# Optimization experiments

Measured on AMD Instinct MI355X. Metric: run time of the kernel, lower is better.

## Reference

```python
import jax, jax.numpy as jnp
import numpy as np

N, DIN = 8192, 768
DH1, DO1 = 64, 64
DH2, DO2 = 32, 64


def setup_inputs() -> dict:
    key = jax.random.key(0)
    ks = jax.random.split(key, 12)
    s = lambda *sh: 0.02
    inp = {
        "X": jax.random.normal(ks[0], (N, DIN), jnp.float32),
        "A": jax.random.randint(ks[1], (N, N), 0, 2, jnp.int32),
        # GAT layer 1: W (din->dh), a (2dh), W2 (dh->dout) + bias
        "W1": jax.random.normal(ks[2], (DIN, DH1), jnp.float32) * 0.02,
        "a1": jax.random.normal(ks[3], (2 * DH1,), jnp.float32) * 0.02,
        "W21": jax.random.normal(ks[4], (DH1, DO1), jnp.float32) * 0.02,
        "b21": jnp.zeros((DO1,), jnp.float32),
        # GAT layer 2
        "Wg2": jax.random.normal(ks[5], (DO1, DH2), jnp.float32) * 0.02,
        "a2": jax.random.normal(ks[6], (2 * DH2,), jnp.float32) * 0.02,
        "W22": jax.random.normal(ks[7], (DH2, DO2), jnp.float32) * 0.02,
        "b22": jnp.zeros((DO2,), jnp.float32),
        # MLP head: 64 -> 64 -> 2
        "M1": jax.random.normal(ks[8], (DO2, 64), jnp.float32) * 0.02,
        "bm1": jnp.zeros((64,), jnp.float32),
        "M2": jax.random.normal(ks[9], (64, 2), jnp.float32) * 0.02,
        "bm2": jnp.zeros((2,), jnp.float32),
    }
    return inp


def _tiny_gat(X, A, W, a, W2, b2):
    # H = X @ W; e_ij = a . [H_i, H_j] = H_i@a_src + H_j@a_dst (same math,
    # no N x N x 2dh intermediate)
    H = X @ W                      # [N, dh]
    dh = W.shape[1]
    e = (H @ a[:dh])[:, None] + (H @ a[dh:])[None, :]   # [N, N]
    e = jnp.where(A == 0, jnp.float32(-1e9), e)
    alpha = jax.nn.softmax(e, axis=1)                   # softmax over neighbors j
    Z = alpha @ H                                       # [N, dh]
    return jax.nn.elu(Z @ W2 + b2)


def reference(X, A, W1, a1, W21, b21, Wg2, a2, W22, b22, M1, bm1, M2, bm2):
    Z = _tiny_gat(X, A, W1, a1, W21, b21)    # [N, 64]
    Z = _tiny_gat(Z, A, Wg2, a2, W22, b22)   # [N, 64]
    g = Z.mean(axis=0)                       # [64]
    h = jax.nn.relu(g @ M1 + bm1)
    return h @ M2 + bm2                      # [2]
```

## Files before the change

### kernel.cpp

```cpp
#include <hip/hip_runtime.h>


#define NN 8192

typedef __attribute__((ext_vector_type(8))) short s16x8;
typedef __attribute__((ext_vector_type(4))) float f32x4;
union V16 { uint4 u; s16x8 s; };

static constexpr size_t OFF_WBITS = 0;
static constexpr size_t OFF_GT1H  = (size_t)8 << 20;
static constexpr size_t OFF_GT1L  = (size_t)9 << 20;
static constexpr size_t OFF_U1    = (size_t)10 << 20;
static constexpr size_t OFF_DEN1  = ((size_t)10 << 20) + 32 * 1024;
static constexpr size_t OFF_GT2H  = ((size_t)10 << 20) + 128 * 1024;
static constexpr size_t OFF_GT2L  = ((size_t)10 << 20) + 896 * 1024;
static constexpr size_t OFF_GPART = ((size_t)11 << 20) + 768 * 1024;
static constexpr size_t OFF_NUMP  = (size_t)12 << 20;
static constexpr size_t OFF_WTAH  = (size_t)44 << 20;
static constexpr size_t OFF_WTAL  = ((size_t)44 << 20) + 128 * 1024;
static constexpr size_t OFF_DP    = (size_t)45 << 20;

__device__ __forceinline__ float elu_f(float x) {
    return x > 0.f ? x : expm1f(x);
}
__device__ __forceinline__ unsigned int bf16_rne(float x) {
    unsigned int u = __float_as_uint(x);
    return (u + 0x7FFFu + ((u >> 16) & 1u)) >> 16;
}
__device__ __forceinline__ unsigned int split_pack(float g) {
    unsigned int hi = bf16_rne(g);
    float fhi = __uint_as_float(hi << 16);
    unsigned int lo = bf16_rne(g - fhi);
    return (hi << 16) | lo;
}
__device__ __forceinline__ void split3(float f, unsigned int& h, unsigned int& m,
                                       unsigned int& l) {
    h = bf16_rne(f);
    float fh = __uint_as_float(h << 16);
    float r1 = f - fh;
    m = bf16_rne(r1);
    float fm = __uint_as_float(m << 16);
    l = bf16_rne(r1 - fm);
}
__device__ __forceinline__ unsigned int bits2bf(unsigned int b2) {
    return (b2 & 1u) * 0x3F80u + (b2 & 2u) * 0x1FC00000u;
}

__global__ __launch_bounds__(256) void k_wsetup(const float* __restrict__ W1,
                                                unsigned int* __restrict__ WtAh,
                                                unsigned int* __restrict__ WtAl) {
    const int t = blockIdx.x * 256 + threadIdx.x;
    const int tile = t >> 6, lane = t & 63;
    const int mt = tile / 24, kt = tile % 24;
    const int feat = mt * 16 + (lane & 15), quad = lane >> 4;
    uint4 hv, lv;
    unsigned int h0, l0, h1, l1;
#define WQ(Q, F)                                                        \
    {                                                                   \
        int k0 = kt * 32 + quad * 8 + 2 * Q;                            \
        float w0 = W1[(size_t)k0 * 64 + feat];                          \
        float w1 = W1[(size_t)(k0 + 1) * 64 + feat];                    \
        h0 = bf16_rne(w0); l0 = bf16_rne(w0 - __uint_as_float(h0 << 16));\
        h1 = bf16_rne(w1); l1 = bf16_rne(w1 - __uint_as_float(h1 << 16));\
        hv.F = h0 | (h1 << 16);                                         \
        lv.F = l0 | (l1 << 16);                                         \
    }
    WQ(0, x) WQ(1, y) WQ(2, z) WQ(3, w)
#undef WQ
    size_t base = (size_t)((mt * 24 + kt) * 64 + lane) * 4;
    *(uint4*)(WtAh + base) = hv;
    *(uint4*)(WtAl + base) = lv;
}

__global__ __launch_bounds__(256) void k_xw1m(const float* __restrict__ X,
                                              const unsigned int* __restrict__ WtAh,
                                              const unsigned int* __restrict__ WtAl,
                                              float* __restrict__ Dp) {
    const int tid = threadIdx.x, wv = tid >> 6, lane = tid & 63;
    const int n = lane & 15, quad = lane >> 4;
    const int node = blockIdx.x * 64 + wv * 16 + n;
    const int ntg = blockIdx.x * 4 + wv;
    const int ks = blockIdx.y;
    f32x4 acc[4];
#pragma unroll
    for (int mt = 0; mt < 4; ++mt) acc[mt] = (f32x4){0.f, 0.f, 0.f, 0.f};
    const float4* X4 = (const float4*)X;
    for (int kk = 0; kk < 6; ++kk) {
        const int kt = ks * 6 + kk;
        float4 x01 = X4[(size_t)node * 192 + kt * 8 + quad * 2];
        float4 x23 = X4[(size_t)node * 192 + kt * 8 + quad * 2 + 1];
        float xf[8] = {x01.x, x01.y, x01.z, x01.w, x23.x, x23.y, x23.z, x23.w};
        V16 bh, bm, bl;
        unsigned int* bhp = (unsigned int*)&bh.u;
        unsigned int* bmp = (unsigned int*)&bm.u;
        unsigned int* blp = (unsigned int*)&bl.u;
#pragma unroll
        for (int q = 0; q < 4; ++q) {
            unsigned int h0, m0, l0, h1, m1, l1;
            split3(xf[2 * q], h0, m0, l0);
            split3(xf[2 * q + 1], h1, m1, l1);
            bhp[q] = h0 | (h1 << 16);
            bmp[q] = m0 | (m1 << 16);
            blp[q] = l0 | (l1 << 16);
        }
#pragma unroll
        for (int mt = 0; mt < 4; ++mt) {
            size_t base = (size_t)((mt * 24 + kt) * 64 + lane) * 4;
            V16 awh, awl;
            awh.u = *(const uint4*)(WtAh + base);
            awl.u = *(const uint4*)(WtAl + base);
            acc[mt] = __builtin_amdgcn_mfma_f32_16x16x32_bf16(awh.s, bh.s, acc[mt], 0, 0, 0);
            acc[mt] = __builtin_amdgcn_mfma_f32_16x16x32_bf16(awh.s, bm.s, acc[mt], 0, 0, 0);
            acc[mt] = __builtin_amdgcn_mfma_f32_16x16x32_bf16(awh.s, bl.s, acc[mt], 0, 0, 0);
            acc[mt] = __builtin_amdgcn_mfma_f32_16x16x32_bf16(awl.s, bh.s, acc[mt], 0, 0, 0);
            acc[mt] = __builtin_amdgcn_mfma_f32_16x16x32_bf16(awl.s, bm.s, acc[mt], 0, 0, 0);
        }
    }
#pragma unroll
    for (int mt = 0; mt < 4; ++mt)
        *(f32x4*)&Dp[(size_t)(((ks * 4 + mt) * 512 + ntg) * 64 + lane) * 4] = acc[mt];
}

__global__ __launch_bounds__(256) void k_xcomb(const float* __restrict__ Dp,
                                               const float* __restrict__ a1,
                                               unsigned int* __restrict__ Gt1h,
                                               unsigned int* __restrict__ Gt1l,
                                               float* __restrict__ u1) {
    __shared__ float Hsh[64][33];
    __shared__ float us[32];
    const int tid = threadIdx.x;
    if (tid < 128) {
        const int ntl = tid >> 6, lane = tid & 63;
        const int n = lane & 15, quad = lane >> 4;
        const int ntg = blockIdx.x * 2 + ntl;
        float dpart = 0.f;
#pragma unroll
        for (int mt = 0; mt < 4; ++mt) {
            float v[4] = {0.f, 0.f, 0.f, 0.f};
#pragma unroll
            for (int ksp = 0; ksp < 4; ++ksp) {
                const float* p = &Dp[(size_t)(((ksp * 4 + mt) * 512 + ntg) * 64 + lane) * 4];
                v[0] += p[0]; v[1] += p[1]; v[2] += p[2]; v[3] += p[3];
            }
#pragma unroll
            for (int r = 0; r < 4; ++r) {
                int feat = mt * 16 + quad * 4 + r;
                Hsh[feat][ntl * 16 + n] = v[r];
                dpart += v[r] * a1[64 + feat];
            }
        }
        dpart += __shfl_xor(dpart, 16);
        dpart += __shfl_xor(dpart, 32);
        float uu = expf(dpart);
        if (lane < 16) {
            us[ntl * 16 + lane] = uu;
            u1[blockIdx.x * 32 + ntl * 16 + lane] = uu;
        }
    }
    __syncthreads();
    {
        const int mt = tid >> 6, lane = tid & 63;
        const int feat = mt * 16 + (lane & 15), quad = lane >> 4;
        uint4 hv, lv;
        unsigned int g0, g1;
#define PACK_Q(Q, FX)                                                   \
        {                                                               \
            int j0 = quad * 8 + 2 * Q;                                  \
            g0 = split_pack(us[j0] * Hsh[feat][j0]);                    \
            g1 = split_pack(us[j0 + 1] * Hsh[feat][j0 + 1]);            \
            hv.FX = (g0 >> 16) | (g1 & 0xFFFF0000u);                    \
            lv.FX = (g0 & 0xFFFFu) | (g1 << 16);                        \
        }
        PACK_Q(0, x) PACK_Q(1, y) PACK_Q(2, z) PACK_Q(3, w)
#undef PACK_Q
        size_t base = ((size_t)(mt * 256 + blockIdx.x) * 64 + lane) * 4;
        *(uint4*)(Gt1h + base) = hv;
        *(uint4*)(Gt1l + base) = lv;
    }
}

__global__ __launch_bounds__(256) void k_pack(const int* __restrict__ A,
                                              const float* __restrict__ u1,
                                              unsigned int* __restrict__ Wb32,
                                              float* __restrict__ den1) {
    __shared__ unsigned short msh[8][512];
    const int tid = threadIdx.x, wv = tid >> 6, lane = tid & 63;
    const int row0 = blockIdx.x * 8;
    float dsum0 = 0.f, dsum1 = 0.f;
    const int r0 = row0 + wv * 2, r1 = r0 + 1;
    for (int c = 0; c < 8; ++c) {
        const int j = c * 1024 + lane * 16;
        const int4* A0 = (const int4*)(A + (size_t)r0 * NN + j);
        const int4* A1 = (const int4*)(A + (size_t)r1 * NN + j);
        const float4* U4 = (const float4*)(u1 + j);
        int4 a0 = A0[0], a1 = A0[1], a2 = A0[2], a3 = A0[3];
        int4 b0 = A1[0], b1 = A1[1], b2 = A1[2], b3 = A1[3];
        float4 u0 = U4[0], u4 = U4[1], u8 = U4[2], uc = U4[3];
        unsigned int m0 = 0, m1 = 0;
#define DO4(AV, BV, UV, SH)                                            \
        m0 |= ((AV.x != 0) << (SH)) | ((AV.y != 0) << (SH + 1)) |      \
              ((AV.z != 0) << (SH + 2)) | ((AV.w != 0) << (SH + 3));   \
        m1 |= ((BV.x != 0) << (SH)) | ((BV.y != 0) << (SH + 1)) |      \
              ((BV.z != 0) << (SH + 2)) | ((BV.w != 0) << (SH + 3));   \
        dsum0 += (AV.x != 0 ? UV.x : 0.f) + (AV.y != 0 ? UV.y : 0.f) + \
                 (AV.z != 0 ? UV.z : 0.f) + (AV.w != 0 ? UV.w : 0.f);  \
        dsum1 += (BV.x != 0 ? UV.x : 0.f) + (BV.y != 0 ? UV.y : 0.f) + \
                 (BV.z != 0 ? UV.z : 0.f) + (BV.w != 0 ? UV.w : 0.f);
        DO4(a0, b0, u0, 0) DO4(a1, b1, u4, 4) DO4(a2, b2, u8, 8) DO4(a3, b3, uc, 12)
#undef DO4
        msh[wv * 2 + 0][c * 64 + lane] = (unsigned short)m0;
        msh[wv * 2 + 1][c * 64 + lane] = (unsigned short)m1;
    }
#pragma unroll
    for (int off = 32; off; off >>= 1) {
        dsum0 += __shfl_down(dsum0, off);
        dsum1 += __shfl_down(dsum1, off);
    }
    if (lane == 0) { den1[r0] = dsum0; den1[r1] = dsum1; }
    __syncthreads();
    {
        const int r = tid >> 5, i = tid & 31;
        const uint4* src = (const uint4*)&msh[r][0];
        uint4* dst = (uint4*)(Wb32 + (size_t)(row0 + r) * 256);
        dst[i] = src[i];
        dst[i + 32] = src[i + 32];
    }
}

__global__ __launch_bounds__(256) void k_attn1(const unsigned int* __restrict__ Wb32,
                                               const unsigned int* __restrict__ Gt1h,
                                               const unsigned int* __restrict__ Gt1l,
                                               float* __restrict__ num1p) {
    __shared__ unsigned int bw[64 * 20];
    const int tid = threadIdx.x, wv = tid >> 6, lane = tid & 63;
    const int node0 = blockIdx.x * 64;
    const int kt0 = blockIdx.y * 16;
    {
        const int r = tid >> 2, part = tid & 3;
        const uint4* src = (const uint4*)(Wb32 + (size_t)(node0 + r) * 256 + kt0 + part * 4);
        *(uint4*)&bw[r * 20 + part * 4] = src[0];
    }
    __syncthreads();
    const int n = lane & 15, quad = lane >> 4;
    const int mt = wv;
    f32x4 acc[4];
#pragma unroll
    for (int nt = 0; nt < 4; ++nt) acc[nt] = (f32x4){0.f, 0.f, 0.f, 0.f};
#pragma unroll 4
    for (int ks = 0; ks < 16; ++ks) {
        size_t base = ((size_t)(mt * 256 + kt0 + ks) * 64 + lane) * 4;
        V16 ah, al;
        ah.u = *(const uint4*)(Gt1h + base);
        al.u = *(const uint4*)(Gt1l + base);
#pragma unroll
        for (int nt = 0; nt < 4; ++nt) {
            unsigned int by8 = (bw[(nt * 16 + n) * 20 + ks] >> (quad * 8)) & 0xFFu;
            V16 bf;
            bf.u = make_uint4(bits2bf(by8), bits2bf(by8 >> 2),
                              bits2bf(by8 >> 4), bits2bf(by8 >> 6));
            acc[nt] = __builtin_amdgcn_mfma_f32_16x16x32_bf16(ah.s, bf.s, acc[nt], 0, 0, 0);
            acc[nt] = __builtin_amdgcn_mfma_f32_16x16x32_bf16(al.s, bf.s, acc[nt], 0, 0, 0);
        }
    }
    const int s = blockIdx.y;
#pragma unroll
    for (int nt = 0; nt < 4; ++nt) {
        const int node = node0 + nt * 16 + n;
        *(f32x4*)&num1p[((size_t)s * NN + node) * 64 + mt * 16 + quad * 4] = acc[nt];
    }
}

__global__ __launch_bounds__(512) void k_ep1(const float* __restrict__ num1p,
                                             const float* __restrict__ den1,
                                             const float* __restrict__ W21,
                                             const float* __restrict__ b21,
                                             const float* __restrict__ Wg2,
                                             const float* __restrict__ a2,
                                             unsigned int* __restrict__ Gt2h,
                                             unsigned int* __restrict__ Gt2l) {
    __shared__ float w21sh[64 * 64];
    __shared__ float wg2sh[64 * 32];
    __shared__ float zsh[8][64];
    __shared__ float osh[8][64];
    __shared__ unsigned int g2sh[32][33];
    __shared__ unsigned int u2sh[32];
    const int tid = threadIdx.x, wv = tid >> 6, lane = tid & 63;
    const int node0 = blockIdx.x * 32;
    {
        const float4* s4 = (const float4*)W21;
        float4* d4 = (float4*)w21sh;
        d4[tid] = s4[tid];
        d4[tid + 512] = s4[tid + 512];
        ((float4*)wg2sh)[tid] = ((const float4*)Wg2)[tid];
    }
    const float bb = b21[lane];
    const int l32 = lane & 31;
    const float a2v = (lane < 32) ? a2[32 + l32] : 0.f;
    __syncthreads();
    for (int it = 0; it < 4; ++it) {
        const int node = node0 + wv * 4 + it;
        float sacc = 0.f;
#pragma unroll
        for (int sp = 0; sp < 16; ++sp)
            sacc += num1p[((size_t)sp * NN + node) * 64 + lane];
        zsh[wv][lane] = sacc / den1[node];
        __builtin_amdgcn_wave_barrier();
        float o0 = 0.f, o1 = 0.f, o2 = 0.f, o3 = 0.f;
        for (int c = 0; c < 64; c += 4) {
            o0 += zsh[wv][c + 0] * w21sh[(c + 0) * 64 + lane];
            o1 += zsh[wv][c + 1] * w21sh[(c + 1) * 64 + lane];
            o2 += zsh[wv][c + 2] * w21sh[(c + 2) * 64 + lane];
            o3 += zsh[wv][c + 3] * w21sh[(c + 3) * 64 + lane];
        }
        float o = elu_f(bb + ((o0 + o1) + (o2 + o3)));
        osh[wv][lane] = o;
        __builtin_amdgcn_wave_barrier();
        float h0 = 0.f, h1 = 0.f;
        for (int c = 0; c < 64; c += 2) {
            h0 += osh[wv][c + 0] * wg2sh[(c + 0) * 32 + l32];
            h1 += osh[wv][c + 1] * wg2sh[(c + 1) * 32 + l32];
        }
        float hval = h0 + h1;
        float pp = hval * a2v;
#pragma unroll
        for (int off = 32; off; off >>= 1) pp += __shfl_down(pp, off);
        float d2 = __shfl(pp, 0);
        float uu = expf(d2);
        const int nodeloc = wv * 4 + it;
        if (lane == 0) u2sh[nodeloc] = split_pack(uu);
        if (lane < 32) g2sh[l32][nodeloc] = split_pack(uu * hval);
    }
    __syncthreads();
    if (tid < 192) {
        const int mt = tid >> 6, lane2 = tid & 63;
        const int ml = lane2 & 15, quad = lane2 >> 4;
        uint4 hv, lv;
        unsigned int g0, g1;
#define PACK_Q(Q, F)                                                   \
        {                                                              \
            int j0 = quad * 8 + 2 * Q;                                 \
            if (mt < 2) { g0 = g2sh[mt * 16 + ml][j0];                 \
                          g1 = g2sh[mt * 16 + ml][j0 + 1]; }           \
            else if (ml == 0) { g0 = u2sh[j0]; g1 = u2sh[j0 + 1]; }    \
            else { g0 = 0; g1 = 0; }                                   \
            hv.F = (g0 >> 16) | (g1 & 0xFFFF0000u);                    \
            lv.F = (g0 & 0xFFFFu) | (g1 << 16);                        \
        }
        PACK_Q(0, x) PACK_Q(1, y) PACK_Q(2, z) PACK_Q(3, w)
#undef PACK_Q
        size_t base = ((size_t)(mt * 256 + blockIdx.x) * 64 + lane2) * 4;
        *(uint4*)(Gt2h + base) = hv;
        *(uint4*)(Gt2l + base) = lv;
    }
}

__global__ __launch_bounds__(256) void k_attn2(const unsigned int* __restrict__ Wb32,
                                               const unsigned int* __restrict__ Gt2h,
                                               const unsigned int* __restrict__ Gt2l,
                                               float* __restrict__ num2p) {
    __shared__ unsigned int bw[64 * 20];
    const int tid = threadIdx.x, wv = tid >> 6, lane = tid & 63;
    const int node0 = blockIdx.x * 64;
    const int kt0 = blockIdx.y * 16;
    {
        const int r = tid >> 2, part = tid & 3;
        const uint4* src = (const uint4*)(Wb32 + (size_t)(node0 + r) * 256 + kt0 + part * 4);
        *(uint4*)&bw[r * 20 + part * 4] = src[0];
    }
    __syncthreads();
    if (wv == 3) return;
    const int n = lane & 15, quad = lane >> 4;
    const int mt = wv;
    f32x4 acc[4];
#pragma unroll
    for (int nt = 0; nt < 4; ++nt) acc[nt] = (f32x4){0.f, 0.f, 0.f, 0.f};
#pragma unroll 4
    for (int ks = 0; ks < 16; ++ks) {
        size_t base = ((size_t)(mt * 256 + kt0 + ks) * 64 + lane) * 4;
        V16 ah, al;
        ah.u = *(const uint4*)(Gt2h + base);
        al.u = *(const uint4*)(Gt2l + base);
#pragma unroll
        for (int nt = 0; nt < 4; ++nt) {
            unsigned int by8 = (bw[(nt * 16 + n) * 20 + ks] >> (quad * 8)) & 0xFFu;
            V16 bf;
            bf.u = make_uint4(bits2bf(by8), bits2bf(by8 >> 2),
                              bits2bf(by8 >> 4), bits2bf(by8 >> 6));
            acc[nt] = __builtin_amdgcn_mfma_f32_16x16x32_bf16(ah.s, bf.s, acc[nt], 0, 0, 0);
            acc[nt] = __builtin_amdgcn_mfma_f32_16x16x32_bf16(al.s, bf.s, acc[nt], 0, 0, 0);
        }
    }
    const int s = blockIdx.y;
#pragma unroll
    for (int nt = 0; nt < 4; ++nt) {
        const int node = node0 + nt * 16 + n;
        *(f32x4*)&num2p[((size_t)s * NN + node) * 48 + mt * 16 + quad * 4] = acc[nt];
    }
}

__global__ __launch_bounds__(512) void k_ep2(const float* __restrict__ num2p,
                                             const float* __restrict__ W22,
                                             const float* __restrict__ b22,
                                             float* __restrict__ gpart) {
    __shared__ float w22sh[32 * 64];
    __shared__ float zsh[8][32];
    __shared__ float gsh[8][64];
    const int tid = threadIdx.x, wv = tid >> 6, lane = tid & 63;
    ((float4*)w22sh)[tid] = ((const float4*)W22)[tid];
    const float bb = b22[lane];
    __syncthreads();
    const int row = blockIdx.x * 8 + wv;
    float val = 0.f;
    if (lane < 33) {
#pragma unroll
        for (int sp = 0; sp < 16; ++sp)
            val += num2p[((size_t)sp * NN + row) * 48 + lane];
    }
    float den = __shfl(val, 32);
    if (lane < 32) zsh[wv][lane] = val / den;
    __builtin_amdgcn_wave_barrier();
    float o0 = 0.f, o1 = 0.f;
    for (int c = 0; c < 32; c += 2) {
        o0 += zsh[wv][c + 0] * w22sh[(c + 0) * 64 + lane];
        o1 += zsh[wv][c + 1] * w22sh[(c + 1) * 64 + lane];
    }
    gsh[wv][lane] = elu_f(bb + o0 + o1);
    __syncthreads();
    if (tid < 64) {
        float s = 0.f;
#pragma unroll
        for (int w = 0; w < 8; ++w) s += gsh[w][tid];
        gpart[(size_t)blockIdx.x * 64 + tid] = s;
    }
}

__global__ __launch_bounds__(256) void k_head(const float* __restrict__ gpart,
                                              const float* __restrict__ M1,
                                              const float* __restrict__ bm1,
                                              const float* __restrict__ M2,
                                              const float* __restrict__ bm2,
                                              float* __restrict__ outp) {
    __shared__ float part[4][64];
    __shared__ float gsh[64];
    __shared__ float hsh[64];
    const int tid = threadIdx.x, col = tid & 63, p = tid >> 6;
    float s = 0.f;
    for (int b = p * 256; b < p * 256 + 256; ++b)
        s += gpart[(size_t)b * 64 + col];
    part[p][col] = s;
    __syncthreads();
    if (tid < 64)
        gsh[tid] = (part[0][tid] + part[1][tid] + part[2][tid] + part[3][tid])
                   * (1.0f / 8192.0f);
    __syncthreads();
    if (tid < 64) {
        float h = bm1[tid];
        for (int c = 0; c < 64; ++c) h += gsh[c] * M1[c * 64 + tid];
        hsh[tid] = h > 0.f ? h : 0.f;
    }
    __syncthreads();
    if (tid < 2) {
        float o = bm2[tid];
        for (int j = 0; j < 64; ++j) o += hsh[j] * M2[j * 2 + tid];
        outp[tid] = o;
    }
}

extern "C" void kernel_launch(void* const* d_in, const int* in_sizes, int n_in,
                              void* d_out, int out_size, void* d_ws, size_t ws_size,
                              hipStream_t stream) {
    const float* X   = (const float*)d_in[0];
    const int*   A   = (const int*)  d_in[1];
    const float* W1  = (const float*)d_in[2];
    const float* a1  = (const float*)d_in[3];
    const float* W21 = (const float*)d_in[4];
    const float* b21 = (const float*)d_in[5];
    const float* Wg2 = (const float*)d_in[6];
    const float* a2  = (const float*)d_in[7];
    const float* W22 = (const float*)d_in[8];
    const float* b22 = (const float*)d_in[9];
    const float* M1  = (const float*)d_in[10];
    const float* bm1 = (const float*)d_in[11];
    const float* M2  = (const float*)d_in[12];
    const float* bm2 = (const float*)d_in[13];
    float* out = (float*)d_out;

    char* ws = (char*)d_ws;
    unsigned int* Wbits = (unsigned int*)(ws + OFF_WBITS);
    unsigned int* Gt1h  = (unsigned int*)(ws + OFF_GT1H);
    unsigned int* Gt1l  = (unsigned int*)(ws + OFF_GT1L);
    unsigned int* Gt2h  = (unsigned int*)(ws + OFF_GT2H);
    unsigned int* Gt2l  = (unsigned int*)(ws + OFF_GT2L);
    unsigned int* WtAh  = (unsigned int*)(ws + OFF_WTAH);
    unsigned int* WtAl  = (unsigned int*)(ws + OFF_WTAL);
    float* Dp    = (float*)(ws + OFF_DP);
    float* u1    = (float*)(ws + OFF_U1);
    float* den1  = (float*)(ws + OFF_DEN1);
    float* gpart = (float*)(ws + OFF_GPART);
    float* nump  = (float*)(ws + OFF_NUMP);

    k_wsetup<<<24, 256, 0, stream>>>(W1, WtAh, WtAl);
    k_xw1m <<<dim3(128, 4), 256, 0, stream>>>(X, WtAh, WtAl, Dp);
    k_xcomb<<<256, 256, 0, stream>>>(Dp, a1, Gt1h, Gt1l, u1);
    k_pack <<<1024, 256, 0, stream>>>(A, u1, Wbits, den1);
    k_attn1<<<dim3(128, 16), 256, 0, stream>>>(Wbits, Gt1h, Gt1l, nump);
    k_ep1  <<<256, 512, 0, stream>>>(nump, den1, W21, b21, Wg2, a2, Gt2h, Gt2l);
    k_attn2<<<dim3(128, 16), 256, 0, stream>>>(Wbits, Gt2h, Gt2l, nump);
    k_ep2  <<<1024, 512, 0, stream>>>(nump, W22, b22, gpart);
    k_head <<<1, 256, 0, stream>>>(gpart, M1, bm1, M2, bm2, out);
}
```

Baseline: 512.4 us.

## Fuse W1 split into xw1m, halve attention K-splits, rebalance pack/epilogue grids

Removes the separate W1 bf16-split setup kernel by having each xw1m block split its W1 slice into shared memory. Attention kernels now process 32 k-tiles per block with 8 splits instead of 16, which halves the partial-sum traffic read by the epilogues. k_pack handles one row per wave across more blocks. k_ep1 uses smaller blocks with more of them, and k_ep2 covers more rows per block. These are many independent retunings at once. They trade a per-block W1 recomputation and lower attention parallelism for fewer launches and less reduction traffic.

```diff
diff --git a/kernel.cpp b/kernel.cpp
--- a/kernel.cpp
+++ b/kernel.cpp
@@ -16,8 +16,6 @@
 static constexpr size_t OFF_GT2L  = ((size_t)10 << 20) + 896 * 1024;
 static constexpr size_t OFF_GPART = ((size_t)11 << 20) + 768 * 1024;
 static constexpr size_t OFF_NUMP  = (size_t)12 << 20;
-static constexpr size_t OFF_WTAH  = (size_t)44 << 20;
-static constexpr size_t OFF_WTAL  = ((size_t)44 << 20) + 128 * 1024;
 static constexpr size_t OFF_DP    = (size_t)45 << 20;
 
 __device__ __forceinline__ float elu_f(float x) {
@@ -46,49 +44,40 @@
     return (b2 & 1u) * 0x3F80u + (b2 & 2u) * 0x1FC00000u;
 }
 
-__global__ __launch_bounds__(256) void k_wsetup(const float* __restrict__ W1,
-                                                unsigned int* __restrict__ WtAh,
-                                                unsigned int* __restrict__ WtAl) {
-    const int t = blockIdx.x * 256 + threadIdx.x;
-    const int tile = t >> 6, lane = t & 63;
-    const int mt = tile / 24, kt = tile % 24;
-    const int feat = mt * 16 + (lane & 15), quad = lane >> 4;
-    uint4 hv, lv;
-    unsigned int h0, l0, h1, l1;
-#define WQ(Q, F)                                                        \
-    {                                                                   \
-        int k0 = kt * 32 + quad * 8 + 2 * Q;                            \
-        float w0 = W1[(size_t)k0 * 64 + feat];                          \
-        float w1 = W1[(size_t)(k0 + 1) * 64 + feat];                    \
-        h0 = bf16_rne(w0); l0 = bf16_rne(w0 - __uint_as_float(h0 << 16));\
-        h1 = bf16_rne(w1); l1 = bf16_rne(w1 - __uint_as_float(h1 << 16));\
-        hv.F = h0 | (h1 << 16);                                         \
-        lv.F = l0 | (l1 << 16);                                         \
-    }
-    WQ(0, x) WQ(1, y) WQ(2, z) WQ(3, w)
-#undef WQ
-    size_t base = (size_t)((mt * 24 + kt) * 64 + lane) * 4;
-    *(uint4*)(WtAh + base) = hv;
-    *(uint4*)(WtAl + base) = lv;
-}
-
 __global__ __launch_bounds__(256) void k_xw1m(const float* __restrict__ X,
-                                              const unsigned int* __restrict__ WtAh,
-                                              const unsigned int* __restrict__ WtAl,
+                                              const float* __restrict__ W1,
                                               float* __restrict__ Dp) {
+    __shared__ unsigned int fh[6144];
+    __shared__ unsigned int fl[6144];
     const int tid = threadIdx.x, wv = tid >> 6, lane = tid & 63;
+    const int ks = blockIdx.y;
+    for (int i = tid; i < 6144; i += 256) {
+        const int feat = i & 63, kp = i >> 6;
+        const int kg = ks * 192 + 2 * kp;
+        float w0 = W1[(size_t)kg * 64 + feat];
+        float w1 = W1[(size_t)(kg + 1) * 64 + feat];
+        unsigned int h0 = bf16_rne(w0);
+        unsigned int l0 = bf16_rne(w0 - __uint_as_float(h0 << 16));
+        unsigned int h1 = bf16_rne(w1);
+        unsigned int l1 = bf16_rne(w1 - __uint_as_float(h1 << 16));
+        const int mt = feat >> 4, n = feat & 15;
+        const int ktl = kp >> 4, rem = kp & 15, quad = rem >> 2, q = rem & 3;
+        const int idx = ((mt * 6 + ktl) * 64 + quad * 16 + n) * 4 + q;
+        fh[idx] = h0 | (h1 << 16);
+        fl[idx] = l0 | (l1 << 16);
+    }
+    __syncthreads();
     const int n = lane & 15, quad = lane >> 4;
     const int node = blockIdx.x * 64 + wv * 16 + n;
     const int ntg = blockIdx.x * 4 + wv;
-    const int ks = blockIdx.y;
     f32x4 acc[4];
 #pragma unroll
     for (int mt = 0; mt < 4; ++mt) acc[mt] = (f32x4){0.f, 0.f, 0.f, 0.f};
     const float4* X4 = (const float4*)X;
     for (int kk = 0; kk < 6; ++kk) {
-        const int kt = ks * 6 + kk;
-        float4 x01 = X4[(size_t)node * 192 + kt * 8 + quad * 2];
-        float4 x23 = X4[(size_t)node * 192 + kt * 8 + quad * 2 + 1];
+        const int ktg = ks * 6 + kk;
+        float4 x01 = X4[(size_t)node * 192 + ktg * 8 + quad * 2];
+        float4 x23 = X4[(size_t)node * 192 + ktg * 8 + quad * 2 + 1];
         float xf[8] = {x01.x, x01.y, x01.z, x01.w, x23.x, x23.y, x23.z, x23.w};
         V16 bh, bm, bl;
         unsigned int* bhp = (unsigned int*)&bh.u;
@@ -105,10 +94,10 @@
         }
 #pragma unroll
         for (int mt = 0; mt < 4; ++mt) {
-            size_t base = (size_t)((mt * 24 + kt) * 64 + lane) * 4;
+            const int base = ((mt * 6 + kk) * 64 + lane) * 4;
             V16 awh, awl;
-            awh.u = *(const uint4*)(WtAh + base);
-            awl.u = *(const uint4*)(WtAl + base);
+            awh.u = *(const uint4*)&fh[base];
+            awl.u = *(const uint4*)&fl[base];
             acc[mt] = __builtin_amdgcn_mfma_f32_16x16x32_bf16(awh.s, bh.s, acc[mt], 0, 0, 0);
             acc[mt] = __builtin_amdgcn_mfma_f32_16x16x32_bf16(awh.s, bm.s, acc[mt], 0, 0, 0);
             acc[mt] = __builtin_amdgcn_mfma_f32_16x16x32_bf16(awh.s, bl.s, acc[mt], 0, 0, 0);
@@ -183,47 +172,36 @@
                                               const float* __restrict__ u1,
                                               unsigned int* __restrict__ Wb32,
                                               float* __restrict__ den1) {
-    __shared__ unsigned short msh[8][512];
+    __shared__ unsigned short msh[4][512];
     const int tid = threadIdx.x, wv = tid >> 6, lane = tid & 63;
-    const int row0 = blockIdx.x * 8;
-    float dsum0 = 0.f, dsum1 = 0.f;
-    const int r0 = row0 + wv * 2, r1 = r0 + 1;
+    const int row0 = blockIdx.x * 4;
+    const int row = row0 + wv;
+    float dsum = 0.f;
     for (int c = 0; c < 8; ++c) {
         const int j = c * 1024 + lane * 16;
-        const int4* A0 = (const int4*)(A + (size_t)r0 * NN + j);
-        const int4* A1 = (const int4*)(A + (size_t)r1 * NN + j);
+        const int4* A0 = (const int4*)(A + (size_t)row * NN + j);
         const float4* U4 = (const float4*)(u1 + j);
         int4 a0 = A0[0], a1 = A0[1], a2 = A0[2], a3 = A0[3];
-        int4 b0 = A1[0], b1 = A1[1], b2 = A1[2], b3 = A1[3];
         float4 u0 = U4[0], u4 = U4[1], u8 = U4[2], uc = U4[3];
-        unsigned int m0 = 0, m1 = 0;
-#define DO4(AV, BV, UV, SH)                                            \
+        unsigned int m0 = 0;
+#define DO4(AV, UV, SH)                                                \
         m0 |= ((AV.x != 0) << (SH)) | ((AV.y != 0) << (SH + 1)) |      \
               ((AV.z != 0) << (SH + 2)) | ((AV.w != 0) << (SH + 3));   \
-        m1 |= ((BV.x != 0) << (SH)) | ((BV.y != 0) << (SH + 1)) |      \
-              ((BV.z != 0) << (SH + 2)) | ((BV.w != 0) << (SH + 3));   \
-        dsum0 += (AV.x != 0 ? UV.x : 0.f) + (AV.y != 0 ? UV.y : 0.f) + \
-                 (AV.z != 0 ? UV.z : 0.f) + (AV.w != 0 ? UV.w : 0.f);  \
-        dsum1 += (BV.x != 0 ? UV.x : 0.f) + (BV.y != 0 ? UV.y : 0.f) + \
-                 (BV.z != 0 ? UV.z : 0.f) + (BV.w != 0 ? UV.w : 0.f);
-        DO4(a0, b0, u0, 0) DO4(a1, b1, u4, 4) DO4(a2, b2, u8, 8) DO4(a3, b3, uc, 12)
+        dsum += (AV.x != 0 ? UV.x : 0.f) + (AV.y != 0 ? UV.y : 0.f) +  \
+                (AV.z != 0 ? UV.z : 0.f) + (AV.w != 0 ? UV.w : 0.f);
+        DO4(a0, u0, 0) DO4(a1, u4, 4) DO4(a2, u8, 8) DO4(a3, uc, 12)
 #undef DO4
-        msh[wv * 2 + 0][c * 64 + lane] = (unsigned short)m0;
-        msh[wv * 2 + 1][c * 64 + lane] = (unsigned short)m1;
-    }
-#pragma unroll
-    for (int off = 32; off; off >>= 1) {
-        dsum0 += __shfl_down(dsum0, off);
-        dsum1 += __shfl_down(dsum1, off);
-    }
-    if (lane == 0) { den1[r0] = dsum0; den1[r1] = dsum1; }
+        msh[wv][c * 64 + lane] = (unsigned short)m0;
+    }
+#pragma unroll
+    for (int off = 32; off; off >>= 1) dsum += __shfl_down(dsum, off);
+    if (lane == 0) den1[row] = dsum;
     __syncthreads();
     {
-        const int r = tid >> 5, i = tid & 31;
+        const int r = tid >> 6, i = tid & 63;
         const uint4* src = (const uint4*)&msh[r][0];
         uint4* dst = (uint4*)(Wb32 + (size_t)(row0 + r) * 256);
         dst[i] = src[i];
-        dst[i + 32] = src[i + 32];
     }
 }
 
@@ -231,14 +209,16 @@
                                                const unsigned int* __restrict__ Gt1h,
                                                const unsigned int* __restrict__ Gt1l,
                                                float* __restrict__ num1p) {
-    __shared__ unsigned int bw[64 * 20];
+    __shared__ unsigned int bw[64 * 36];
     const int tid = threadIdx.x, wv = tid >> 6, lane = tid & 63;
     const int node0 = blockIdx.x * 64;
-    const int kt0 = blockIdx.y * 16;
+    const int kt0 = blockIdx.y * 32;
     {
         const int r = tid >> 2, part = tid & 3;
-        const uint4* src = (const uint4*)(Wb32 + (size_t)(node0 + r) * 256 + kt0 + part * 4);
-        *(uint4*)&bw[r * 20 + part * 4] = src[0];
+        const uint4* src = (const uint4*)(Wb32 + (size_t)(node0 + r) * 256 + kt0 + part * 8);
+        uint4 v0 = src[0], v1 = src[1];
+        *(uint4*)&bw[r * 36 + part * 8] = v0;
+        *(uint4*)&bw[r * 36 + part * 8 + 4] = v1;
     }
     __syncthreads();
     const int n = lane & 15, quad = lane >> 4;
@@ -247,14 +227,14 @@
 #pragma unroll
     for (int nt = 0; nt < 4; ++nt) acc[nt] = (f32x4){0.f, 0.f, 0.f, 0.f};
 #pragma unroll 4
-    for (int ks = 0; ks < 16; ++ks) {
+    for (int ks = 0; ks < 32; ++ks) {
         size_t base = ((size_t)(mt * 256 + kt0 + ks) * 64 + lane) * 4;
         V16 ah, al;
         ah.u = *(const uint4*)(Gt1h + base);
         al.u = *(const uint4*)(Gt1l + base);
 #pragma unroll
         for (int nt = 0; nt < 4; ++nt) {
-            unsigned int by8 = (bw[(nt * 16 + n) * 20 + ks] >> (quad * 8)) & 0xFFu;
+            unsigned int by8 = (bw[(nt * 16 + n) * 36 + ks] >> (quad * 8)) & 0xFFu;
             V16 bf;
             bf.u = make_uint4(bits2bf(by8), bits2bf(by8 >> 2),
                               bits2bf(by8 >> 4), bits2bf(by8 >> 6));
@@ -270,7 +250,7 @@
     }
 }
 
-__global__ __launch_bounds__(512) void k_ep1(const float* __restrict__ num1p,
+__global__ __launch_bounds__(256) void k_ep1(const float* __restrict__ num1p,
                                              const float* __restrict__ den1,
                                              const float* __restrict__ W21,
                                              const float* __restrict__ b21,
@@ -280,45 +260,54 @@
                                              unsigned int* __restrict__ Gt2l) {
     __shared__ float w21sh[64 * 64];
     __shared__ float wg2sh[64 * 32];
-    __shared__ float zsh[8][64];
-    __shared__ float osh[8][64];
-    __shared__ unsigned int g2sh[32][33];
-    __shared__ unsigned int u2sh[32];
+    __shared__ float zsh[4][64];
+    __shared__ float osh[4][64];
+    __shared__ unsigned int g2sh[32][9];
+    __shared__ unsigned int u2sh[8];
     const int tid = threadIdx.x, wv = tid >> 6, lane = tid & 63;
-    const int node0 = blockIdx.x * 32;
+    const int node0 = blockIdx.x * 8;
     {
         const float4* s4 = (const float4*)W21;
         float4* d4 = (float4*)w21sh;
         d4[tid] = s4[tid];
+        d4[tid + 256] = s4[tid + 256];
         d4[tid + 512] = s4[tid + 512];
+        d4[tid + 768] = s4[tid + 768];
         ((float4*)wg2sh)[tid] = ((const float4*)Wg2)[tid];
+        ((float4*)wg2sh)[tid + 256] = ((const float4*)Wg2)[tid + 256];
     }
     const float bb = b21[lane];
     const int l32 = lane & 31;
     const float a2v = (lane < 32) ? a2[32 + l32] : 0.f;
     __syncthreads();
-    for (int it = 0; it < 4; ++it) {
-        const int node = node0 + wv * 4 + it;
+    for (int it = 0; it < 2; ++it) {
+        const int node = node0 + wv * 2 + it;
         float sacc = 0.f;
 #pragma unroll
-        for (int sp = 0; sp < 16; ++sp)
+        for (int sp = 0; sp < 8; ++sp)
             sacc += num1p[((size_t)sp * NN + node) * 64 + lane];
         zsh[wv][lane] = sacc / den1[node];
         __builtin_amdgcn_wave_barrier();
-        float o0 = 0.f, o1 = 0.f, o2 = 0.f, o3 = 0.f;
-        for (int c = 0; c < 64; c += 4) {
-            o0 += zsh[wv][c + 0] * w21sh[(c + 0) * 64 + lane];
-            o1 += zsh[wv][c + 1] * w21sh[(c + 1) * 64 + lane];
-            o2 += zsh[wv][c + 2] * w21sh[(c + 2) * 64 + lane];
-            o3 += zsh[wv][c + 3] * w21sh[(c + 3) * 64 + lane];
-        }
-        float o = elu_f(bb + ((o0 + o1) + (o2 + o3)));
+        const float4* zv = (const float4*)&zsh[wv][0];
+        float o0 = 0.f, o1 = 0.f;
+#pragma unroll 4
+        for (int c4 = 0; c4 < 16; ++c4) {
+            float4 z4 = zv[c4];
+            const int c = c4 * 4;
+            o0 += z4.x * w21sh[(c + 0) * 64 + lane] + z4.y * w21sh[(c + 1) * 64 + lane];
+            o1 += z4.z * w21sh[(c + 2) * 64 + lane] + z4.w * w21sh[(c + 3) * 64 + lane];
+        }
+        float o = elu_f(bb + o0 + o1);
         osh[wv][lane] = o;
         __builtin_amdgcn_wave_barrier();
+        const float4* ov = (const float4*)&osh[wv][0];
         float h0 = 0.f, h1 = 0.f;
-        for (int c = 0; c < 64; c += 2) {
-            h0 += osh[wv][c + 0] * wg2sh[(c + 0) * 32 + l32];
-            h1 += osh[wv][c + 1] * wg2sh[(c + 1) * 32 + l32];
+#pragma unroll 4
+        for (int c4 = 0; c4 < 16; ++c4) {
+            float4 o4 = ov[c4];
+            const int c = c4 * 4;
+            h0 += o4.x * wg2sh[(c + 0) * 32 + l32] + o4.y * wg2sh[(c + 1) * 32 + l32];
+            h1 += o4.z * wg2sh[(c + 2) * 32 + l32] + o4.w * wg2sh[(c + 3) * 32 + l32];
         }
         float hval = h0 + h1;
         float pp = hval * a2v;
@@ -326,19 +315,20 @@
         for (int off = 32; off; off >>= 1) pp += __shfl_down(pp, off);
         float d2 = __shfl(pp, 0);
         float uu = expf(d2);
-        const int nodeloc = wv * 4 + it;
+        const int nodeloc = wv * 2 + it;
         if (lane == 0) u2sh[nodeloc] = split_pack(uu);
         if (lane < 32) g2sh[l32][nodeloc] = split_pack(uu * hval);
     }
     __syncthreads();
-    if (tid < 192) {
-        const int mt = tid >> 6, lane2 = tid & 63;
-        const int ml = lane2 & 15, quad = lane2 >> 4;
+    if (tid < 48) {
+        const int mt = tid >> 4, ml = tid & 15;
+        const int quad_w = blockIdx.x & 3, kt = blockIdx.x >> 2;
+        const int lane2 = quad_w * 16 + ml;
         uint4 hv, lv;
         unsigned int g0, g1;
 #define PACK_Q(Q, F)                                                   \
         {                                                              \
-            int j0 = quad * 8 + 2 * Q;                                 \
+            int j0 = 2 * Q;                                            \
             if (mt < 2) { g0 = g2sh[mt * 16 + ml][j0];                 \
                           g1 = g2sh[mt * 16 + ml][j0 + 1]; }           \
             else if (ml == 0) { g0 = u2sh[j0]; g1 = u2sh[j0 + 1]; }    \
@@ -348,7 +338,7 @@
         }
         PACK_Q(0, x) PACK_Q(1, y) PACK_Q(2, z) PACK_Q(3, w)
 #undef PACK_Q
-        size_t base = ((size_t)(mt * 256 + blockIdx.x) * 64 + lane2) * 4;
+        size_t base = ((size_t)(mt * 256 + kt) * 64 + lane2) * 4;
         *(uint4*)(Gt2h + base) = hv;
         *(uint4*)(Gt2l + base) = lv;
     }
@@ -358,14 +348,16 @@
                                                const unsigned int* __restrict__ Gt2h,
                                                const unsigned int* __restrict__ Gt2l,
                                                float* __restrict__ num2p) {
-    __shared__ unsigned int bw[64 * 20];
+    __shared__ unsigned int bw[64 * 36];
     const int tid = threadIdx.x, wv = tid >> 6, lane = tid & 63;
     const int node0 = blockIdx.x * 64;
-    const int kt0 = blockIdx.y * 16;
+    const int kt0 = blockIdx.y * 32;
     {
         const int r = tid >> 2, part = tid & 3;
-        const uint4* src = (const uint4*)(Wb32 + (size_t)(node0 + r) * 256 + kt0 + part * 4);
-        *(uint4*)&bw[r * 20 + part * 4] = src[0];
+        const uint4* src = (const uint4*)(Wb32 + (size_t)(node0 + r) * 256 + kt0 + part * 8);
+        uint4 v0 = src[0], v1 = src[1];
+        *(uint4*)&bw[r * 36 + part * 8] = v0;
+        *(uint4*)&bw[r * 36 + part * 8 + 4] = v1;
     }
     __syncthreads();
     if (wv == 3) return;
@@ -375,14 +367,14 @@
 #pragma unroll
     for (int nt = 0; nt < 4; ++nt) acc[nt] = (f32x4){0.f, 0.f, 0.f, 0.f};
 #pragma unroll 4
-    for (int ks = 0; ks < 16; ++ks) {
+    for (int ks = 0; ks < 32; ++ks) {
         size_t base = ((size_t)(mt * 256 + kt0 + ks) * 64 + lane) * 4;
         V16 ah, al;
         ah.u = *(const uint4*)(Gt2h + base);
         al.u = *(const uint4*)(Gt2l + base);
 #pragma unroll
         for (int nt = 0; nt < 4; ++nt) {
-            unsigned int by8 = (bw[(nt * 16 + n) * 20 + ks] >> (quad * 8)) & 0xFFu;
+            unsigned int by8 = (bw[(nt * 16 + n) * 36 + ks] >> (quad * 8)) & 0xFFu;
             V16 bf;
             bf.u = make_uint4(bits2bf(by8), bits2bf(by8 >> 2),
                               bits2bf(by8 >> 4), bits2bf(by8 >> 6));
@@ -409,22 +401,31 @@
     ((float4*)w22sh)[tid] = ((const float4*)W22)[tid];
     const float bb = b22[lane];
     __syncthreads();
-    const int row = blockIdx.x * 8 + wv;
-    float val = 0.f;
-    if (lane < 33) {
-#pragma unroll
-        for (int sp = 0; sp < 16; ++sp)
-            val += num2p[((size_t)sp * NN + row) * 48 + lane];
-    }
-    float den = __shfl(val, 32);
-    if (lane < 32) zsh[wv][lane] = val / den;
-    __builtin_amdgcn_wave_barrier();
-    float o0 = 0.f, o1 = 0.f;
-    for (int c = 0; c < 32; c += 2) {
-        o0 += zsh[wv][c + 0] * w22sh[(c + 0) * 64 + lane];
-        o1 += zsh[wv][c + 1] * w22sh[(c + 1) * 64 + lane];
-    }
-    gsh[wv][lane] = elu_f(bb + o0 + o1);
+    float greg = 0.f;
+    for (int it = 0; it < 4; ++it) {
+        const int row = blockIdx.x * 32 + wv * 4 + it;
+        float val = 0.f;
+        if (lane < 33) {
+#pragma unroll
+            for (int sp = 0; sp < 8; ++sp)
+                val += num2p[((size_t)sp * NN + row) * 48 + lane];
+        }
+        float den = __shfl(val, 32);
+        if (lane < 32) zsh[wv][lane] = val / den;
+        __builtin_amdgcn_wave_barrier();
+        const float4* zv = (const float4*)&zsh[wv][0];
+        float o0 = 0.f, o1 = 0.f;
+#pragma unroll 4
+        for (int c4 = 0; c4 < 8; ++c4) {
+            float4 z4 = zv[c4];
+            const int c = c4 * 4;
+            o0 += z4.x * w22sh[(c + 0) * 64 + lane] + z4.y * w22sh[(c + 1) * 64 + lane];
+            o1 += z4.z * w22sh[(c + 2) * 64 + lane] + z4.w * w22sh[(c + 3) * 64 + lane];
+        }
+        greg += elu_f(bb + o0 + o1);
+        __builtin_amdgcn_wave_barrier();
+    }
+    gsh[wv][lane] = greg;
     __syncthreads();
     if (tid < 64) {
         float s = 0.f;
@@ -445,7 +446,7 @@
     __shared__ float hsh[64];
     const int tid = threadIdx.x, col = tid & 63, p = tid >> 6;
     float s = 0.f;
-    for (int b = p * 256; b < p * 256 + 256; ++b)
+    for (int b = p * 64; b < p * 64 + 64; ++b)
         s += gpart[(size_t)b * 64 + col];
     part[p][col] = s;
     __syncthreads();
@@ -491,21 +492,18 @@
     unsigned int* Gt1l  = (unsigned int*)(ws + OFF_GT1L);
     unsigned int* Gt2h  = (unsigned int*)(ws + OFF_GT2H);
     unsigned int* Gt2l  = (unsigned int*)(ws + OFF_GT2L);
-    unsigned int* WtAh  = (unsigned int*)(ws + OFF_WTAH);
-    unsigned int* WtAl  = (unsigned int*)(ws + OFF_WTAL);
     float* Dp    = (float*)(ws + OFF_DP);
     float* u1    = (float*)(ws + OFF_U1);
     float* den1  = (float*)(ws + OFF_DEN1);
     float* gpart = (float*)(ws + OFF_GPART);
     float* nump  = (float*)(ws + OFF_NUMP);
 
-    k_wsetup<<<24, 256, 0, stream>>>(W1, WtAh, WtAl);
-    k_xw1m <<<dim3(128, 4), 256, 0, stream>>>(X, WtAh, WtAl, Dp);
+    k_xw1m <<<dim3(128, 4), 256, 0, stream>>>(X, W1, Dp);
     k_xcomb<<<256, 256, 0, stream>>>(Dp, a1, Gt1h, Gt1l, u1);
-    k_pack <<<1024, 256, 0, stream>>>(A, u1, Wbits, den1);
-    k_attn1<<<dim3(128, 16), 256, 0, stream>>>(Wbits, Gt1h, Gt1l, nump);
-    k_ep1  <<<256, 512, 0, stream>>>(nump, den1, W21, b21, Wg2, a2, Gt2h, Gt2l);
-    k_attn2<<<dim3(128, 16), 256, 0, stream>>>(Wbits, Gt2h, Gt2l, nump);
-    k_ep2  <<<1024, 512, 0, stream>>>(nump, W22, b22, gpart);
+    k_pack <<<2048, 256, 0, stream>>>(A, u1, Wbits, den1);
+    k_attn1<<<dim3(128, 8), 256, 0, stream>>>(Wbits, Gt1h, Gt1l, nump);
+    k_ep1  <<<1024, 256, 0, stream>>>(nump, den1, W21, b21, Wg2, a2, Gt2h, Gt2l);
+    k_attn2<<<dim3(128, 8), 256, 0, stream>>>(Wbits, Gt2h, Gt2l, nump);
+    k_ep2  <<<256, 512, 0, stream>>>(nump, W22, b22, gpart);
     k_head <<<1, 256, 0, stream>>>(gpart, M1, bm1, M2, bm2, out);
 }
```

Result: no change. 519.5 us (+1.4%).
